# Kernel optimization log

Measured on AMD Instinct MI355X. Metric: run time of the kernel, lower is better.

The kernel has to match this reference:

```python
import jax, jax.numpy as jnp
import numpy as np
from jax import lax

HEADS = 8
DN = ('NCHW', 'OIHW', 'NCHW')


def setup_inputs() -> dict:
    key = jax.random.key(0)
    ks = jax.random.split(key, 7)
    B, C, H, W = 1, 256, 64, 64
    s = lambda k, shape, fan: jax.random.normal(k, shape, jnp.float32) / np.sqrt(fan)
    return {
        'x': jax.random.normal(ks[0], (B, C, H, W), jnp.float32),
        'w_qkv_pw': s(ks[1], (3 * C, C, 1, 1), C),
        'b_qkv_pw': jnp.zeros((3 * C,), jnp.float32),
        'w_qkv_dw': s(ks[2], (3 * C, 1, 11, 11), 121),
        'b_qkv_dw': jnp.zeros((3 * C,), jnp.float32),
        'w_lin': s(ks[3], (C, C, 1, 1), C),
        'b_lin': jnp.zeros((C,), jnp.float32),
    }


def reference(x, w_qkv_pw, b_qkv_pw, w_qkv_dw, b_qkv_dw, w_lin, b_lin):
    B, C, H, W = x.shape
    d = C // HEADS
    temp = float(int(np.sqrt(d)))  # matches int(math.sqrt(C // head)) in source

    # QKV: 1x1 conv then 11x11 depthwise conv (groups = 3C), padding 5
    qkv = lax.conv_general_dilated(x, w_qkv_pw, (1, 1), 'VALID', dimension_numbers=DN)
    qkv = qkv + b_qkv_pw[None, :, None, None]
    qkv = lax.conv_general_dilated(qkv, w_qkv_dw, (1, 1), [(5, 5), (5, 5)],
                                   dimension_numbers=DN, feature_group_count=3 * C)
    qkv = qkv + b_qkv_dw[None, :, None, None]

    q, k, v = jnp.split(qkv, 3, axis=1)  # each [B, C, H, W]
    N = H * W
    q = q.reshape(B, HEADS, d, N)
    k = k.reshape(B, HEADS, d, N)
    v = v.reshape(B, HEADS, d, N)

    # attn = softmax(q^T k / temp) over keys; [B, h, N, N]
    scores = jnp.einsum('bhdn,bhdm->bhnm', q, k) / temp
    attn = jax.nn.softmax(scores, axis=-1)
    out = jnp.einsum('bhnm,bhdm->bhdn', attn, v)  # [B, h, d, N]
    new_x = out.reshape(B, C, H, W)

    proj = lax.conv_general_dilated(new_x, w_lin, (1, 1), 'VALID', dimension_numbers=DN)
    proj = proj + b_lin[None, :, None, None]
    return jax.nn.relu(proj) + x
```

## Files before the change

kernel.cpp:

```cpp
#include <hip/hip_runtime.h>


typedef _Float16 f16;
typedef __fp16 hf16x2 __attribute__((ext_vector_type(2)));
typedef _Float16 f16x4 __attribute__((ext_vector_type(4)));
typedef _Float16 f16x8 __attribute__((ext_vector_type(8)));
typedef float f32x4 __attribute__((ext_vector_type(4)));

#define HW 4096
#define NC 256

#if __has_builtin(__builtin_amdgcn_exp2f)
#define EXP2(x) __builtin_amdgcn_exp2f(x)
#else
#define EXP2(x) exp2f(x)
#endif

static __device__ __forceinline__ f32x4 mfma16(f16x8 a, f16x8 b, f32x4 c) {
  return __builtin_amdgcn_mfma_f32_16x16x32_f16(a, b, c, 0, 0, 0);
}

static __device__ __forceinline__ void gload16(const void* g, void* l) {
  __builtin_amdgcn_global_load_lds(
      (const __attribute__((address_space(1))) unsigned int*)g,
      (__attribute__((address_space(3))) unsigned int*)l, 16, 0, 0);
}

__global__ __launch_bounds__(256) void k_prep(
    const float* __restrict__ x, f16* __restrict__ xt,
    const float* __restrict__ wpw, const float* __restrict__ wlin,
    f16* __restrict__ wpw_h, f16* __restrict__ wlin_h,
    int* __restrict__ kmaxd_bits) {
  __shared__ float t[32][33];
  int b = blockIdx.x;
  if (b < 1024) {
    int bc = b >> 7;
    int bp = b & 127;
    int tx = threadIdx.x & 31, ty = threadIdx.x >> 5;
#pragma unroll
    for (int i = 0; i < 4; i++) {
      int c = bc * 32 + ty + i * 8;
      t[ty + i * 8][tx] = x[c * HW + bp * 32 + tx];
    }
    __syncthreads();
#pragma unroll
    for (int i = 0; i < 4; i++) {
      int p = bp * 32 + ty + i * 8;
      xt[p * NC + bc * 32 + tx] = (f16)t[tx][ty + i * 8];
    }
  } else {
    int i = (b - 1024) * 256 + threadIdx.x;
    if (i < 256) kmaxd_bits[i] = 0;
    for (int idx = i; idx < 3 * NC * NC; idx += 32768)
      wpw_h[idx] = (f16)wpw[idx];
    for (int idx = i; idx < NC * NC; idx += 32768)
      wlin_h[idx] = (f16)wlin[idx];
  }
}

__global__ __launch_bounds__(256) void k_gemm_qkv(
    const f16* __restrict__ w, const f16* __restrict__ xt,
    const float* __restrict__ bias, f16* __restrict__ out) {
  __shared__ f16 lds_b[64 * 256];
  int bm = blockIdx.x >> 6;
  int bn = blockIdx.x & 63;
  int tid = threadIdx.x;
  int wave = tid >> 6, lane = tid & 63;
  int r = lane & 15, g = lane >> 4;
  int m0 = bm * 128 + wave * 32;
  int n0 = bn * 64;
#pragma unroll
  for (int round = 0; round < 8; ++round) {
    int idx = round * 256 + tid;
    int row = idx >> 5;
    int sd = (idx & 31) ^ (row & 7);
    gload16(xt + (n0 + row) * 256 + sd * 8,
            (char*)lds_b + round * 4096 + wave * 1024);
  }
  __syncthreads();
  f32x4 acc[2][4] = {};
  for (int kk = 0; kk < NC; kk += 32) {
    f16x8 a0 = *(const f16x8*)&w[(m0 + r) * NC + kk + g * 8];
    f16x8 a1 = *(const f16x8*)&w[(m0 + 16 + r) * NC + kk + g * 8];
    int sb = (kk >> 3) + g;
#pragma unroll
    for (int nt = 0; nt < 4; nt++) {
      int row = nt * 16 + r;
      f16x8 bfr = *(const f16x8*)((char*)lds_b + row * 512 +
                                  ((sb ^ (row & 7)) * 16));
      acc[0][nt] = mfma16(a0, bfr, acc[0][nt]);
      acc[1][nt] = mfma16(a1, bfr, acc[1][nt]);
    }
  }
#pragma unroll
  for (int mg = 0; mg < 2; mg++) {
    int mbase = m0 + mg * 16 + g * 4;
    float bj[4];
#pragma unroll
    for (int j = 0; j < 4; j++) bj[j] = bias[mbase + j];
#pragma unroll
    for (int nt = 0; nt < 4; nt++)
#pragma unroll
      for (int j = 0; j < 4; j++)
        out[(mbase + j) * HW + n0 + nt * 16 + r] =
            (f16)(acc[mg][nt][j] + bj[j]);
  }
}

__global__ __launch_bounds__(256) void k_dwconv(
    const f16* __restrict__ qkv, const float* __restrict__ wdw,
    const float* __restrict__ bdw, f16* __restrict__ q_nm,
    f16* __restrict__ k_nm, f16* __restrict__ v_cm,
    int* __restrict__ kmaxd_bits) {
  __shared__ float img[42 * 74];
  __shared__ float wgt[121];
  int b = blockIdx.x;
  int c = b >> 1, half = b & 1;
  int y0 = half * 32;
  int tid = threadIdx.x;
  for (int i = tid; i < 420; i += 256) {
    int row = i / 10, cc = i - row * 10;
    img[row * 74 + (cc < 5 ? cc : 64 + cc)] = 0.f;
  }
  const f16x8 zv = {};
  for (int task = tid; task < 336; task += 256) {
    int row = task >> 3, ch = task & 7;
    int y = y0 + row - 5;
    f16x8 v = ((unsigned)y < 64u)
                  ? *(const f16x8*)&qkv[c * HW + y * 64 + ch * 8]
                  : zv;
    float* dst = &img[row * 74 + 5 + ch * 8];
#pragma unroll
    for (int j = 0; j < 8; j++) dst[j] = (float)v[j];
  }
  for (int i = tid; i < 121; i += 256) wgt[i] = wdw[c * 121 + i];
  __syncthreads();
  float bias = bdw[c];
  int px0 = half * 2048 + tid * 8;
  int yl = tid >> 3;
  int x0 = (tid & 7) * 8;
  float acc[8] = {};
#pragma unroll
  for (int ky = 0; ky < 11; ky++) {
    const float* rp = &img[(yl + ky) * 74 + x0];
    float rv[18];
#pragma unroll
    for (int t = 0; t < 18; t++) rv[t] = rp[t];
#pragma unroll
    for (int kx = 0; kx < 11; kx++) {
      float wv = wgt[ky * 11 + kx];
#pragma unroll
      for (int p = 0; p < 8; p++) acc[p] = fmaf(rv[kx + p], wv, acc[p]);
    }
  }
  if (c < 256) {
    int h = c >> 5, d = c & 31;
#pragma unroll
    for (int p = 0; p < 8; p++)
      q_nm[(h * HW + px0 + p) * 32 + d] =
          (f16)((acc[p] + bias) * 0.28853900817779268f);
  } else if (c < 512) {
    int cc = c - 256;
    int h = cc >> 5, d = cc & 31;
    float m = 0.f;
#pragma unroll
    for (int p = 0; p < 8; p++) {
      float kv = acc[p] + bias;
      k_nm[(h * HW + px0 + p) * 32 + d] = (f16)kv;
      m = fmaxf(m, fabsf(kv));
    }
    __syncthreads();
    img[tid] = m;
    __syncthreads();
    for (int off = 128; off > 0; off >>= 1) {
      if (tid < off) img[tid] = fmaxf(img[tid], img[tid + off]);
      __syncthreads();
    }
    if (tid == 0) atomicMax(&kmaxd_bits[cc], __float_as_int(img[0]));
  } else {
    int cc = c - 512;
#pragma unroll
    for (int p = 0; p < 8; p++)
      v_cm[cc * HW + px0 + p] = (f16)(acc[p] + bias);
  }
}

__global__ __launch_bounds__(512, 4) void k_attn(
    const f16* __restrict__ q_nm, const f16* __restrict__ k_nm,
    const f16* __restrict__ v_cm, const int* __restrict__ kmaxd_bits,
    f16* __restrict__ o_part, float* __restrict__ l_part) {
  __shared__ f16 lds_k[4][2048];
  __shared__ f16 lds_v[4][2048];
  int bid = blockIdx.x;
  int h = bid & 7, kq = (bid >> 3) & 3, qt = bid >> 5;
  int tid = threadIdx.x;
  int wv = tid >> 6, lane = tid & 63;
  int r = lane & 15, g = lane >> 4;
  int n_base = qt * 256 + wv * 32;
  int m_lo = kq << 10;
  const f16* qh = q_nm + h * (HW * 32);
  const f16* kh = k_nm + h * (HW * 32) + m_lo * 32;
  const f16* vh = v_cm + h * (32 * HW) + m_lo;

  f16x8 bq0 = *(const f16x8*)&qh[(n_base + r) * 32 + g * 8];
  f16x8 bq1 = *(const f16x8*)&qh[(n_base + 16 + r) * 32 + g * 8];
  const float* kmd = (const float*)kmaxd_bits + h * 32 + g * 8;
  f32x4 kd0 = *(const f32x4*)kmd;
  f32x4 kd1 = *(const f32x4*)(kmd + 4);
  float ba = 0.f, bb = 0.f;
#pragma unroll
  for (int j = 0; j < 4; j++) {
    ba = fmaf(fabsf((float)bq0[j]), kd0[j], ba);
    ba = fmaf(fabsf((float)bq0[4 + j]), kd1[j], ba);
    bb = fmaf(fabsf((float)bq1[j]), kd0[j], bb);
    bb = fmaf(fabsf((float)bq1[4 + j]), kd1[j], bb);
  }
  ba += __shfl_xor(ba, 16);
  ba += __shfl_xor(ba, 32);
  bb += __shfl_xor(bb, 16);
  bb += __shfl_xor(bb, 32);
  float mCa = 13.9f - ba;
  float mCb = 13.9f - bb;
  f32x4 cinitA = {mCa, mCa, mCa, mCa};
  f32x4 cinitB = {mCb, mCb, mCb, mCb};
  int pr = ((r & 12) << 1) | (r & 3);
  f32x4 accA0 = {0.f, 0.f, 0.f, 0.f}, accA1 = {0.f, 0.f, 0.f, 0.f};
  f32x4 accB0 = {0.f, 0.f, 0.f, 0.f}, accB1 = {0.f, 0.f, 0.f, 0.f};
  float La = 0.f, Lb = 0.f;

  int l4 = lane >> 2, l3 = lane & 3;
  int kc = (wv & 3) * 16 + l4;
  int ku = (kc >> 3) & 3;
  const f16* kg_base = kh + kc * 32 + (l3 ^ ku) * 8;
  int t2v = (tid >= 256) ? tid - 256 : 0;
  int vd = t2v >> 3;
  int vkk = ((t2v & 7) ^ (vd & 7)) * 8;
  const f16* vg_base = vh + vd * HW + vkk;
  f16* kdst = &lds_k[0][0] + (wv & 3) * 512;
  f16* vdst = &lds_v[0][0] + (t2v >> 6) * 512;

  int u = r >> 2;
  int kslot = ((g ^ u) & 3) * 16;
  int ak0_off = pr * 64 + kslot;
  int ak1_off = (pr + 4) * 64 + kslot;
  int vb_off0 = (r * 128 + g * 16) ^ ((r & 7) << 4);
  int vb_off1 = (r * 128 + 64 + g * 16) ^ ((r & 7) << 4);

  __builtin_amdgcn_s_waitcnt(0);
  if (wv < 4) {
    gload16(kg_base, kdst);
    gload16(kg_base + 2048, kdst + 2048);
  } else {
    gload16(vg_base, vdst);
    gload16(vg_base + 64, vdst + 2048);
  }

  for (int t = 0; t < 16; ++t) {
    int c2 = (t + 2 <= 15) ? t + 2 : 15;
    int b2 = (t + 2) & 3;
    if (wv < 4)
      gload16(kg_base + c2 * 2048, kdst + b2 * 2048);
    else
      gload16(vg_base + c2 * 64, vdst + b2 * 2048);
    asm volatile("s_waitcnt vmcnt(2)" ::: "memory");
    __builtin_amdgcn_sched_barrier(0);
    __builtin_amdgcn_s_barrier();
    __builtin_amdgcn_sched_barrier(0);
    const char* kb = (const char*)&lds_k[t & 3][0];
    const char* vb = (const char*)&lds_v[t & 3][0];
#pragma unroll
    for (int ks = 0; ks < 2; ++ks) {
      f16x8 ak0 = *(const f16x8*)(kb + ks * 2048 + ak0_off);
      f16x8 ak1 = *(const f16x8*)(kb + ks * 2048 + ak1_off);
      int vo = ks ? vb_off1 : vb_off0;
      f16x8 bv0 = *(const f16x8*)(vb + vo);
      f16x8 bv1 = *(const f16x8*)(vb + vo + 2048);
      __builtin_amdgcn_s_setprio(1);
      f32x4 sA0 = mfma16(ak0, bq0, cinitA);
      f32x4 sA1 = mfma16(ak1, bq0, cinitA);
      f32x4 sB0 = mfma16(ak0, bq1, cinitB);
      f32x4 sB1 = mfma16(ak1, bq1, cinitB);
      __builtin_amdgcn_s_setprio(0);
      float pA[8], pB[8];
#pragma unroll
      for (int j = 0; j < 4; j++) {
        pA[j] = EXP2(sA0[j]);
        pA[4 + j] = EXP2(sA1[j]);
        pB[j] = EXP2(sB0[j]);
        pB[4 + j] = EXP2(sB1[j]);
      }
      La += ((pA[0] + pA[1]) + (pA[2] + pA[3])) +
            ((pA[4] + pA[5]) + (pA[6] + pA[7]));
      Lb += ((pB[0] + pB[1]) + (pB[2] + pB[3])) +
            ((pB[4] + pB[5]) + (pB[6] + pB[7]));
      union { hf16x2 h2[4]; f16x8 v; } uA, uB;
#pragma unroll
      for (int j = 0; j < 4; j++) {
        uA.h2[j] = __builtin_amdgcn_cvt_pkrtz(pA[2 * j], pA[2 * j + 1]);
        uB.h2[j] = __builtin_amdgcn_cvt_pkrtz(pB[2 * j], pB[2 * j + 1]);
      }
      __builtin_amdgcn_s_setprio(1);
      accA0 = mfma16(uA.v, bv0, accA0);
      accA1 = mfma16(uA.v, bv1, accA1);
      accB0 = mfma16(uB.v, bv0, accB0);
      accB1 = mfma16(uB.v, bv1, accB1);
      __builtin_amdgcn_s_setprio(0);
    }
  }
  La += __shfl_xor(La, 16);
  La += __shfl_xor(La, 32);
  Lb += __shfl_xor(Lb, 16);
  Lb += __shfl_xor(Lb, 32);
  float ilA = 1.f / La, ilB = 1.f / Lb;
  f16* op = o_part + ((((size_t)kq * 8 + h) * HW) + n_base) * 32;
#pragma unroll
  for (int j = 0; j < 4; j++) {
    float ija = __shfl(ilA, 4 * g + j);
    float ijb = __shfl(ilB, 4 * g + j);
    op[(4 * g + j) * 32 + r] = (f16)(accA0[j] * ija);
    op[(4 * g + j) * 32 + 16 + r] = (f16)(accA1[j] * ija);
    op[(16 + 4 * g + j) * 32 + r] = (f16)(accB0[j] * ijb);
    op[(16 + 4 * g + j) * 32 + 16 + r] = (f16)(accB1[j] * ijb);
  }
  if (lane < 16) {
    l_part[(((size_t)kq * 8 + h) * HW) + n_base + r] = La;
    l_part[(((size_t)kq * 8 + h) * HW) + n_base + 16 + r] = Lb;
  }
}

__global__ __launch_bounds__(256) void k_gemm_proj(
    const f16* __restrict__ w, const f16* __restrict__ o_part,
    const float* __restrict__ l_part, const float* __restrict__ bias,
    const float* __restrict__ x, float* __restrict__ out) {
  __shared__ f16 lds_b[32 * 256];
  int bm = blockIdx.x >> 7;
  int bn = blockIdx.x & 127;
  int tid = threadIdx.x;
  int wave = tid >> 6, lane = tid & 63;
  int r = lane & 15, g = lane >> 4;
  int m_row = bm * 64 + wave * 16 + r;
  int n0 = bn * 32;
#pragma unroll
  for (int round = 0; round < 4; ++round) {
    int task = round * 256 + tid;
    int row = task >> 5, grp = task & 31;
    int h = grp >> 2, d0 = (grp & 3) * 8;
    size_t rbase = ((size_t)h * HW) + n0 + row;
    float Lq[4];
    f16x8 oq[4];
#pragma unroll
    for (int q = 0; q < 4; q++) {
      Lq[q] = l_part[(size_t)q * 8 * HW + rbase];
      oq[q] = *(const f16x8*)&o_part[((size_t)q * 8 * HW + rbase) * 32 + d0];
    }
    float inv = 1.f / ((Lq[0] + Lq[1]) + (Lq[2] + Lq[3]));
    f16x8 outv;
#pragma unroll
    for (int j = 0; j < 8; j++) {
      float o = 0.f;
#pragma unroll
      for (int q = 0; q < 4; q++) o = fmaf((float)oq[q][j], Lq[q], o);
      outv[j] = (f16)(o * inv);
    }
    *(f16x8*)((char*)lds_b + row * 512 + ((grp ^ (row & 7)) * 16)) = outv;
  }
  __syncthreads();
  f32x4 acc[2] = {};
  for (int kk = 0; kk < NC; kk += 32) {
    f16x8 a = *(const f16x8*)&w[m_row * NC + kk + g * 8];
    int sb = (kk >> 3) + g;
#pragma unroll
    for (int nt = 0; nt < 2; nt++) {
      int row = nt * 16 + r;
      f16x8 bfr = *(const f16x8*)((char*)lds_b + row * 512 +
                                  ((sb ^ (row & 7)) * 16));
      acc[nt] = mfma16(a, bfr, acc[nt]);
    }
  }
  int mbase = bm * 64 + wave * 16 + g * 4;
  float bj[4];
#pragma unroll
  for (int j = 0; j < 4; j++) bj[j] = bias[mbase + j];
#pragma unroll
  for (int nt = 0; nt < 2; nt++)
#pragma unroll
    for (int j = 0; j < 4; j++) {
      int m = mbase + j, n = n0 + nt * 16 + r;
      float v = fmaxf(acc[nt][j] + bj[j], 0.f) + x[m * HW + n];
      out[m * HW + n] = v;
    }
}

extern "C" void kernel_launch(void* const* d_in, const int* in_sizes, int n_in,
                              void* d_out, int out_size, void* d_ws,
                              size_t ws_size, hipStream_t stream) {
  const float* x = (const float*)d_in[0];
  const float* w_pw = (const float*)d_in[1];
  const float* b_pw = (const float*)d_in[2];
  const float* w_dw = (const float*)d_in[3];
  const float* b_dw = (const float*)d_in[4];
  const float* w_lin = (const float*)d_in[5];
  const float* b_lin = (const float*)d_in[6];
  float* out = (float*)d_out;

  char* ws = (char*)d_ws;
  f16* wpw_h = (f16*)(ws + 0);
  f16* wlin_h = (f16*)(ws + 393216);
  f16* xt = (f16*)(ws + 524288);
  f16* qkv = (f16*)(ws + 2621440);
  f16* q_nm = (f16*)(ws + 15204352);
  f16* k_nm = (f16*)(ws + 17301504);
  f16* v_cm = (f16*)(ws + 19398656);
  int* kmaxd_bits = (int*)(ws + 23724032);
  f16* o_part = (f16*)(ws + 2621440);
  float* l_part = (float*)(ws + 2621440 + 8388608);

  k_prep<<<1152, 256, 0, stream>>>(x, xt, w_pw, w_lin, wpw_h, wlin_h,
                                   kmaxd_bits);
  k_gemm_qkv<<<384, 256, 0, stream>>>(wpw_h, xt, b_pw, qkv);
  k_dwconv<<<1536, 256, 0, stream>>>(qkv, w_dw, b_dw, q_nm, k_nm, v_cm,
                                     kmaxd_bits);
  k_attn<<<512, 512, 0, stream>>>(q_nm, k_nm, v_cm, kmaxd_bits, o_part,
                                  l_part);
  k_gemm_proj<<<512, 256, 0, stream>>>(wlin_h, o_part, l_part, b_lin, x, out);
}
```

Baseline: 74.49 us.

## Fuse prep transpose and weight casts into the QKV and projection GEMMs

Removes the separate k_prep kernel. The QKV GEMM now reads fp32 x directly, transposes and converts it to fp16 into swizzled LDS, and clears kmaxd_bits itself. Both GEMMs now load fp32 weights and convert them to fp16 on the fly. This drops one kernel launch and the xt/weight workspace round-trip. In exchange, each GEMM block does redundant weight conversion and reads wider fp32 data. Every one of the 384 QKV blocks also rewrites kmaxd_bits, a benign duplicate write.

```diff
diff --git a/kernel.cpp b/kernel.cpp
--- a/kernel.cpp
+++ b/kernel.cpp
@@ -26,41 +26,21 @@
       (__attribute__((address_space(3))) unsigned int*)l, 16, 0, 0);
 }
 
-__global__ __launch_bounds__(256) void k_prep(
-    const float* __restrict__ x, f16* __restrict__ xt,
-    const float* __restrict__ wpw, const float* __restrict__ wlin,
-    f16* __restrict__ wpw_h, f16* __restrict__ wlin_h,
+static __device__ __forceinline__ f16x8 load_a_f32(const float* p) {
+  f32x4 lo = *(const f32x4*)p, hi = *(const f32x4*)(p + 4);
+  f16x8 a;
+#pragma unroll
+  for (int j = 0; j < 4; j++) {
+    a[j] = (f16)lo[j];
+    a[4 + j] = (f16)hi[j];
+  }
+  return a;
+}
+
+__global__ __launch_bounds__(256) void k_gemm_qkv(
+    const float* __restrict__ w, const float* __restrict__ x,
+    const float* __restrict__ bias, f16* __restrict__ out,
     int* __restrict__ kmaxd_bits) {
-  __shared__ float t[32][33];
-  int b = blockIdx.x;
-  if (b < 1024) {
-    int bc = b >> 7;
-    int bp = b & 127;
-    int tx = threadIdx.x & 31, ty = threadIdx.x >> 5;
-#pragma unroll
-    for (int i = 0; i < 4; i++) {
-      int c = bc * 32 + ty + i * 8;
-      t[ty + i * 8][tx] = x[c * HW + bp * 32 + tx];
-    }
-    __syncthreads();
-#pragma unroll
-    for (int i = 0; i < 4; i++) {
-      int p = bp * 32 + ty + i * 8;
-      xt[p * NC + bc * 32 + tx] = (f16)t[tx][ty + i * 8];
-    }
-  } else {
-    int i = (b - 1024) * 256 + threadIdx.x;
-    if (i < 256) kmaxd_bits[i] = 0;
-    for (int idx = i; idx < 3 * NC * NC; idx += 32768)
-      wpw_h[idx] = (f16)wpw[idx];
-    for (int idx = i; idx < NC * NC; idx += 32768)
-      wlin_h[idx] = (f16)wlin[idx];
-  }
-}
-
-__global__ __launch_bounds__(256) void k_gemm_qkv(
-    const f16* __restrict__ w, const f16* __restrict__ xt,
-    const float* __restrict__ bias, f16* __restrict__ out) {
   __shared__ f16 lds_b[64 * 256];
   int bm = blockIdx.x >> 6;
   int bn = blockIdx.x & 63;
@@ -69,19 +49,32 @@
   int r = lane & 15, g = lane >> 4;
   int m0 = bm * 128 + wave * 32;
   int n0 = bn * 64;
-#pragma unroll
-  for (int round = 0; round < 8; ++round) {
-    int idx = round * 256 + tid;
-    int row = idx >> 5;
-    int sd = (idx & 31) ^ (row & 7);
-    gload16(xt + (n0 + row) * 256 + sd * 8,
-            (char*)lds_b + round * 4096 + wave * 1024);
+  kmaxd_bits[tid] = 0;
+#pragma unroll
+  for (int round = 0; round < 4; ++round) {
+    int task = round * 256 + tid;
+    int pg = task & 15, cg = task >> 4;
+    int p0 = pg * 4, c0 = cg * 4;
+    f32x4 v[4];
+#pragma unroll
+    for (int cc = 0; cc < 4; cc++)
+      v[cc] = *(const f32x4*)&x[(c0 + cc) * HW + n0 + p0];
+#pragma unroll
+    for (int pp = 0; pp < 4; pp++) {
+      int row = p0 + pp;
+      f16x4 o;
+#pragma unroll
+      for (int cc = 0; cc < 4; cc++) o[cc] = (f16)v[cc][pp];
+      int byteoff =
+          row * 512 + (((c0 >> 3) ^ (row & 7)) << 4) + (c0 & 4) * 2;
+      *(f16x4*)((char*)lds_b + byteoff) = o;
+    }
   }
   __syncthreads();
   f32x4 acc[2][4] = {};
   for (int kk = 0; kk < NC; kk += 32) {
-    f16x8 a0 = *(const f16x8*)&w[(m0 + r) * NC + kk + g * 8];
-    f16x8 a1 = *(const f16x8*)&w[(m0 + 16 + r) * NC + kk + g * 8];
+    f16x8 a0 = load_a_f32(&w[(m0 + r) * NC + kk + g * 8]);
+    f16x8 a1 = load_a_f32(&w[(m0 + 16 + r) * NC + kk + g * 8]);
     int sb = (kk >> 3) + g;
 #pragma unroll
     for (int nt = 0; nt < 4; nt++) {
@@ -329,7 +322,7 @@
 }
 
 __global__ __launch_bounds__(256) void k_gemm_proj(
-    const f16* __restrict__ w, const f16* __restrict__ o_part,
+    const float* __restrict__ w, const f16* __restrict__ o_part,
     const float* __restrict__ l_part, const float* __restrict__ bias,
     const float* __restrict__ x, float* __restrict__ out) {
   __shared__ f16 lds_b[32 * 256];
@@ -367,7 +360,7 @@
   __syncthreads();
   f32x4 acc[2] = {};
   for (int kk = 0; kk < NC; kk += 32) {
-    f16x8 a = *(const f16x8*)&w[m_row * NC + kk + g * 8];
+    f16x8 a = load_a_f32(&w[m_row * NC + kk + g * 8]);
     int sb = (kk >> 3) + g;
 #pragma unroll
     for (int nt = 0; nt < 2; nt++) {
@@ -404,9 +397,6 @@
   float* out = (float*)d_out;
 
   char* ws = (char*)d_ws;
-  f16* wpw_h = (f16*)(ws + 0);
-  f16* wlin_h = (f16*)(ws + 393216);
-  f16* xt = (f16*)(ws + 524288);
   f16* qkv = (f16*)(ws + 2621440);
   f16* q_nm = (f16*)(ws + 15204352);
   f16* k_nm = (f16*)(ws + 17301504);
@@ -415,12 +405,10 @@
   f16* o_part = (f16*)(ws + 2621440);
   float* l_part = (float*)(ws + 2621440 + 8388608);
 
-  k_prep<<<1152, 256, 0, stream>>>(x, xt, w_pw, w_lin, wpw_h, wlin_h,
-                                   kmaxd_bits);
-  k_gemm_qkv<<<384, 256, 0, stream>>>(wpw_h, xt, b_pw, qkv);
+  k_gemm_qkv<<<384, 256, 0, stream>>>(w_pw, x, b_pw, qkv, kmaxd_bits);
   k_dwconv<<<1536, 256, 0, stream>>>(qkv, w_dw, b_dw, q_nm, k_nm, v_cm,
                                      kmaxd_bits);
   k_attn<<<512, 512, 0, stream>>>(q_nm, k_nm, v_cm, kmaxd_bits, o_part,
                                   l_part);
-  k_gemm_proj<<<512, 256, 0, stream>>>(wlin_h, o_part, l_part, b_lin, x, out);
-}
+  k_gemm_proj<<<512, 256, 0, stream>>>(w_lin, o_part, l_part, b_lin, x, out);
+}
```

After: 72.77 us, median of 2. -2.3%, faster.
